# Performance work log

Hardware: AMD Instinct MI355X
Metric: run time of the kernel (lower is better)

Reference implementation:

```python
import jax, jax.numpy as jnp
import numpy as np

B, C, F_IN, F_HID, F_OUT = 256, 4096, 160, 192, 1
EPS = 1e-5


def setup_inputs() -> dict:
    key = jax.random.key(0)
    k1, k2, k3 = jax.random.split(key, 3)
    x = jax.random.normal(k1, (B, C, F_IN), dtype=jnp.float32)
    # MultipleLinear init: N(0, sqrt(2/in_features))
    W1 = jax.random.normal(k2, (C, F_HID, F_IN), dtype=jnp.float32) * np.sqrt(2.0 / F_IN)
    gamma = jnp.ones((C, F_HID), dtype=jnp.float32)
    beta = jnp.zeros((C, F_HID), dtype=jnp.float32)
    W2 = jax.random.normal(k3, (C, F_OUT, F_HID), dtype=jnp.float32) * np.sqrt(2.0 / F_HID)
    b2 = jnp.zeros((C, F_OUT), dtype=jnp.float32)
    return {"x": x, "W1": W1, "gamma": gamma, "beta": beta, "W2": W2, "b2": b2}


def reference(x, W1, gamma, beta, W2, b2):
    # Per-cell grouped linear: [B,C,160] x [C,192,160] -> [B,C,192]
    h = jnp.einsum('bci,coi->bco', x, W1)
    # Training-mode batchnorm over the batch dim, per (cell, feature)
    mean = jnp.mean(h, axis=0)                      # [C,192]
    var = jnp.mean((h - mean) ** 2, axis=0)         # biased variance, [C,192]
    h = (h - mean) * jax.lax.rsqrt(var + EPS) * gamma + beta
    h = jax.nn.relu(h)
    # Final per-cell linear: [B,C,192] x [C,1,192] -> [B,C,1]
    return jnp.einsum('bch,coh->bco', h, W2) + b2
```

## Files before the change

kernel.cpp:

```cpp
#include <hip/hip_runtime.h>
#include <hip/hip_bf16.h>

#define B_DIM 256
#define C_DIM 4096
#define FIN   160
#define FHID  192
#define EPS   1e-5f

#define AST 40
#define BST 40

typedef short  short8  __attribute__((ext_vector_type(8)));
typedef float  floatx4 __attribute__((ext_vector_type(4)));

__device__ __forceinline__ short f2bs(float f) {
  __hip_bfloat16 h = __float2bfloat16(f);
  return *reinterpret_cast<short*>(&h);
}

__device__ __forceinline__ void cvt_store8(short* dst, const float4& v0, const float4& v1) {
  short8 s;
  s[0] = f2bs(v0.x); s[1] = f2bs(v0.y); s[2] = f2bs(v0.z); s[3] = f2bs(v0.w);
  s[4] = f2bs(v1.x); s[5] = f2bs(v1.y); s[6] = f2bs(v1.z); s[7] = f2bs(v1.w);
  *reinterpret_cast<short8*>(dst) = s;
}

__global__ __launch_bounds__(1024) void mlp_fused_kernel(
    const float* __restrict__ x,
    const float* __restrict__ W1,
    const float* __restrict__ gamma,
    const float* __restrict__ beta,
    const float* __restrict__ W2,
    const float* __restrict__ b2,
    float* __restrict__ out)
{
  const int c    = blockIdx.x;
  const int tid  = threadIdx.x;
  const int lane = tid & 63;
  const int wave = tid >> 6;
  const int wr   = wave >> 2;
  const int wc   = wave & 3;
  const int l15  = lane & 15;
  const int lg   = lane >> 4;

  __shared__ __align__(16) short Alds[B_DIM * AST];
  __shared__ __align__(16) short Blds[FHID * BST];
  __shared__ float psum[4][FHID];
  __shared__ float psq [4][FHID];
  __shared__ float scaleS[FHID];
  __shared__ float shiftS[FHID];
  __shared__ float w2S[FHID];
  __shared__ float rowp[4][B_DIM];

  const float* xc  = x  + (size_t)c * FIN;
  const float* w1c = W1 + (size_t)c * FHID * FIN;

  const int  arow = tid >> 2;
  const int  aq   = (tid & 3) * 8;
  const bool bact = tid < 768;

  float4 a0, a1, b0, b1;
  {
    const float* pa = xc + (size_t)arow * (C_DIM * FIN) + aq;
    a0 = *reinterpret_cast<const float4*>(pa);
    a1 = *reinterpret_cast<const float4*>(pa + 4);
    if (bact) {
      const float* pb = w1c + arow * FIN + aq;
      b0 = *reinterpret_cast<const float4*>(pb);
      b1 = *reinterpret_cast<const float4*>(pb + 4);
    }
  }

  floatx4 acc[4][3];
  #pragma unroll
  for (int mt = 0; mt < 4; ++mt)
    #pragma unroll
    for (int nt = 0; nt < 3; ++nt)
      acc[mt][nt] = (floatx4)(0.f);

  for (int kc = 0; kc < 5; ++kc) {
    cvt_store8(&Alds[arow * AST + aq], a0, a1);
    if (bact) cvt_store8(&Blds[arow * BST + aq], b0, b1);
    __syncthreads();

    if (kc < 4) {
      const int k0 = (kc + 1) * 32;
      const float* pa = xc + (size_t)arow * (C_DIM * FIN) + k0 + aq;
      a0 = *reinterpret_cast<const float4*>(pa);
      a1 = *reinterpret_cast<const float4*>(pa + 4);
      if (bact) {
        const float* pb = w1c + arow * FIN + k0 + aq;
        b0 = *reinterpret_cast<const float4*>(pb);
        b1 = *reinterpret_cast<const float4*>(pb + 4);
      }
    }

    short8 af[4], bf[3];
    #pragma unroll
    for (int mt = 0; mt < 4; ++mt) {
      const int row = wr * 64 + mt * 16 + l15;
      af[mt] = *reinterpret_cast<const short8*>(&Alds[row * AST + lg * 8]);
    }
    #pragma unroll
    for (int nt = 0; nt < 3; ++nt) {
      const int row = wc * 48 + nt * 16 + l15;
      bf[nt] = *reinterpret_cast<const short8*>(&Blds[row * BST + lg * 8]);
    }
    #pragma unroll
    for (int mt = 0; mt < 4; ++mt)
      #pragma unroll
      for (int nt = 0; nt < 3; ++nt)
        acc[mt][nt] = __builtin_amdgcn_mfma_f32_16x16x32_bf16(
            af[mt], bf[nt], acc[mt][nt], 0, 0, 0);
    __syncthreads();
  }

  #pragma unroll
  for (int nt = 0; nt < 3; ++nt) {
    float s = 0.f, q = 0.f;
    #pragma unroll
    for (int mt = 0; mt < 4; ++mt)
      #pragma unroll
      for (int r = 0; r < 4; ++r) {
        const float v = acc[mt][nt][r];
        s += v; q += v * v;
      }
    s += __shfl_xor(s, 16); q += __shfl_xor(q, 16);
    s += __shfl_xor(s, 32); q += __shfl_xor(q, 32);
    if (lg == 0) {
      const int col = wc * 48 + nt * 16 + l15;
      psum[wr][col] = s;
      psq [wr][col] = q;
    }
  }
  __syncthreads();

  if (tid < FHID) {
    const float s  = psum[0][tid] + psum[1][tid] + psum[2][tid] + psum[3][tid];
    const float q  = psq [0][tid] + psq [1][tid] + psq [2][tid] + psq [3][tid];
    const float mean = s * (1.f / 256.f);
    const float var  = q * (1.f / 256.f) - mean * mean;
    const float rstd = rsqrtf(var + EPS);
    const float sc   = rstd * gamma[(size_t)c * FHID + tid];
    scaleS[tid] = sc;
    shiftS[tid] = beta[(size_t)c * FHID + tid] - mean * sc;
    w2S[tid]    = W2[(size_t)c * FHID + tid];
  }
  __syncthreads();

  #pragma unroll
  for (int mt = 0; mt < 4; ++mt) {
    #pragma unroll
    for (int r = 0; r < 4; ++r) {
      float p = 0.f;
      #pragma unroll
      for (int nt = 0; nt < 3; ++nt) {
        const int col = wc * 48 + nt * 16 + l15;
        float v = acc[mt][nt][r] * scaleS[col] + shiftS[col];
        v = fmaxf(v, 0.f);
        p += v * w2S[col];
      }
      p += __shfl_xor(p, 1);
      p += __shfl_xor(p, 2);
      p += __shfl_xor(p, 4);
      p += __shfl_xor(p, 8);
      if (l15 == 0) {
        const int row = wr * 64 + mt * 16 + lg * 4 + r;
        rowp[wc][row] = p;
      }
    }
  }
  __syncthreads();

  if (tid < B_DIM) {
    const float o = rowp[0][tid] + rowp[1][tid] + rowp[2][tid] + rowp[3][tid] + b2[c];
    out[(size_t)tid * C_DIM + c] = o;
  }
}

extern "C" void kernel_launch(void* const* d_in, const int* in_sizes, int n_in,
                              void* d_out, int out_size, void* d_ws, size_t ws_size,
                              hipStream_t stream) {
  const float* x     = (const float*)d_in[0];
  const float* W1    = (const float*)d_in[1];
  const float* gamma = (const float*)d_in[2];
  const float* beta  = (const float*)d_in[3];
  const float* W2    = (const float*)d_in[4];
  const float* b2    = (const float*)d_in[5];
  float* out = (float*)d_out;
  mlp_fused_kernel<<<C_DIM, 1024, 0, stream>>>(x, W1, gamma, beta, W2, b2, out);
}
```

Before: 1.204 ms.

## Stage full K dimension in LDS with all global loads issued upfront

Adds a kernel variant that loads the entire 160-wide K slice of x and W1 for a cell into about 160 KB of dynamic LDS in one burst. Each thread issues 20 vector loads before converting to bf16, then runs all five MFMA k-steps without intermediate barriers. This aims to raise memory-level parallelism and remove the per-chunk sync/load serialization of the double-buffered loop. The cost is that the LDS footprint limits a CU to one 1024-thread block, where the old kernel could fit two. The old kernel is kept as a fallback if the shared-memory attribute or the launch fails.

New measurement: 1.207 ms. Within noise of the previous version (+0.2%).

```diff
diff --git a/kernel.cpp b/kernel.cpp
--- a/kernel.cpp
+++ b/kernel.cpp
@@ -7,9 +7,6 @@
 #define FHID  192
 #define EPS   1e-5f
 
-#define AST 40
-#define BST 40
-
 typedef short  short8  __attribute__((ext_vector_type(8)));
 typedef float  floatx4 __attribute__((ext_vector_type(4)));
 
@@ -25,7 +22,170 @@
   *reinterpret_cast<short8*>(dst) = s;
 }
 
-__global__ __launch_bounds__(1024) void mlp_fused_kernel(
+#define AST_BIG 168
+#define A_SH (B_DIM * AST_BIG)
+#define B_SH (FHID  * AST_BIG)
+#define SMEM_BYTES (A_SH*2 + B_SH*2 + (8*FHID + 3*FHID + 4*B_DIM)*4)
+
+__global__ __launch_bounds__(1024) void mlp_fused_big(
+    const float* __restrict__ x,
+    const float* __restrict__ W1,
+    const float* __restrict__ gamma,
+    const float* __restrict__ beta,
+    const float* __restrict__ W2,
+    const float* __restrict__ b2,
+    float* __restrict__ out)
+{
+  extern __shared__ __align__(16) char smem[];
+  short* Alds   = reinterpret_cast<short*>(smem);
+  short* Blds   = Alds + A_SH;
+  float* psum   = reinterpret_cast<float*>(smem + (size_t)(A_SH + B_SH) * 2);
+  float* psq    = psum + 4 * FHID;
+  float* scaleS = psq + 4 * FHID;
+  float* shiftS = scaleS + FHID;
+  float* w2S    = shiftS + FHID;
+  float* rowp   = w2S + FHID;
+
+  const int c    = blockIdx.x;
+  const int tid  = threadIdx.x;
+  const int lane = tid & 63;
+  const int wave = tid >> 6;
+  const int wr   = wave >> 2;
+  const int wc   = wave & 3;
+  const int l15  = lane & 15;
+  const int lg   = lane >> 4;
+
+  const float* xc  = x  + (size_t)c * FIN;
+  const float* w1c = W1 + (size_t)c * FHID * FIN;
+
+  const int  r    = tid >> 2;
+  const int  q    = tid & 3;
+  const bool bact = tid < 4 * FHID;
+
+  {
+    const float* pa = xc + (size_t)r * (C_DIM * FIN) + q * 8;
+    const float* pb = w1c + r * FIN + q * 8;
+
+    float4 av[10];
+    float4 bv[10];
+    #pragma unroll
+    for (int j = 0; j < 5; ++j) {
+      av[2*j]   = *reinterpret_cast<const float4*>(pa + j*32);
+      av[2*j+1] = *reinterpret_cast<const float4*>(pa + j*32 + 4);
+    }
+    if (bact) {
+      #pragma unroll
+      for (int j = 0; j < 5; ++j) {
+        bv[2*j]   = *reinterpret_cast<const float4*>(pb + j*32);
+        bv[2*j+1] = *reinterpret_cast<const float4*>(pb + j*32 + 4);
+      }
+    }
+    short* da = Alds + r * AST_BIG + q * 8;
+    #pragma unroll
+    for (int j = 0; j < 5; ++j) cvt_store8(da + j*32, av[2*j], av[2*j+1]);
+    if (bact) {
+      short* db = Blds + r * AST_BIG + q * 8;
+      #pragma unroll
+      for (int j = 0; j < 5; ++j) cvt_store8(db + j*32, bv[2*j], bv[2*j+1]);
+    }
+  }
+  __syncthreads();
+
+  floatx4 acc[4][3];
+  #pragma unroll
+  for (int mt = 0; mt < 4; ++mt)
+    #pragma unroll
+    for (int nt = 0; nt < 3; ++nt)
+      acc[mt][nt] = (floatx4)(0.f);
+
+  const short* aB = Alds + (wr * 64 + l15) * AST_BIG + lg * 8;
+  const short* bB = Blds + (wc * 48 + l15) * AST_BIG + lg * 8;
+
+  #pragma unroll
+  for (int kc = 0; kc < 5; ++kc) {
+    short8 af[4], bf[3];
+    #pragma unroll
+    for (int mt = 0; mt < 4; ++mt)
+      af[mt] = *reinterpret_cast<const short8*>(aB + mt * 16 * AST_BIG + kc * 32);
+    #pragma unroll
+    for (int nt = 0; nt < 3; ++nt)
+      bf[nt] = *reinterpret_cast<const short8*>(bB + nt * 16 * AST_BIG + kc * 32);
+    #pragma unroll
+    for (int mt = 0; mt < 4; ++mt)
+      #pragma unroll
+      for (int nt = 0; nt < 3; ++nt)
+        acc[mt][nt] = __builtin_amdgcn_mfma_f32_16x16x32_bf16(
+            af[mt], bf[nt], acc[mt][nt], 0, 0, 0);
+  }
+
+  #pragma unroll
+  for (int nt = 0; nt < 3; ++nt) {
+    float s = 0.f, qq = 0.f;
+    #pragma unroll
+    for (int mt = 0; mt < 4; ++mt)
+      #pragma unroll
+      for (int rr = 0; rr < 4; ++rr) {
+        const float v = acc[mt][nt][rr];
+        s += v; qq += v * v;
+      }
+    s += __shfl_xor(s, 16); qq += __shfl_xor(qq, 16);
+    s += __shfl_xor(s, 32); qq += __shfl_xor(qq, 32);
+    if (lg == 0) {
+      const int col = wc * 48 + nt * 16 + l15;
+      psum[wr * FHID + col] = s;
+      psq [wr * FHID + col] = qq;
+    }
+  }
+  __syncthreads();
+
+  if (tid < FHID) {
+    const float s  = psum[0*FHID + tid] + psum[1*FHID + tid] + psum[2*FHID + tid] + psum[3*FHID + tid];
+    const float qq = psq [0*FHID + tid] + psq [1*FHID + tid] + psq [2*FHID + tid] + psq [3*FHID + tid];
+    const float mean = s * (1.f / 256.f);
+    const float var  = qq * (1.f / 256.f) - mean * mean;
+    const float rstd = rsqrtf(var + EPS);
+    const float sc   = rstd * gamma[(size_t)c * FHID + tid];
+    scaleS[tid] = sc;
+    shiftS[tid] = beta[(size_t)c * FHID + tid] - mean * sc;
+    w2S[tid]    = W2[(size_t)c * FHID + tid];
+  }
+  __syncthreads();
+
+  #pragma unroll
+  for (int mt = 0; mt < 4; ++mt) {
+    #pragma unroll
+    for (int rr = 0; rr < 4; ++rr) {
+      float p = 0.f;
+      #pragma unroll
+      for (int nt = 0; nt < 3; ++nt) {
+        const int col = wc * 48 + nt * 16 + l15;
+        float v = acc[mt][nt][rr] * scaleS[col] + shiftS[col];
+        v = fmaxf(v, 0.f);
+        p += v * w2S[col];
+      }
+      p += __shfl_xor(p, 1);
+      p += __shfl_xor(p, 2);
+      p += __shfl_xor(p, 4);
+      p += __shfl_xor(p, 8);
+      if (l15 == 0) {
+        const int row = wr * 64 + mt * 16 + lg * 4 + rr;
+        rowp[wc * B_DIM + row] = p;
+      }
+    }
+  }
+  __syncthreads();
+
+  if (tid < B_DIM) {
+    const float o = rowp[0*B_DIM + tid] + rowp[1*B_DIM + tid]
+                  + rowp[2*B_DIM + tid] + rowp[3*B_DIM + tid] + b2[c];
+    out[(size_t)tid * C_DIM + c] = o;
+  }
+}
+
+#define AST 40
+#define BST 40
+
+__global__ __launch_bounds__(1024) void mlp_fused_small(
     const float* __restrict__ x,
     const float* __restrict__ W1,
     const float* __restrict__ gamma,
@@ -117,29 +277,29 @@
 
   #pragma unroll
   for (int nt = 0; nt < 3; ++nt) {
-    float s = 0.f, q = 0.f;
-    #pragma unroll
-    for (int mt = 0; mt < 4; ++mt)
-      #pragma unroll
-      for (int r = 0; r < 4; ++r) {
-        const float v = acc[mt][nt][r];
-        s += v; q += v * v;
-      }
-    s += __shfl_xor(s, 16); q += __shfl_xor(q, 16);
-    s += __shfl_xor(s, 32); q += __shfl_xor(q, 32);
+    float s = 0.f, qv = 0.f;
+    #pragma unroll
+    for (int mt = 0; mt < 4; ++mt)
+      #pragma unroll
+      for (int rr = 0; rr < 4; ++rr) {
+        const float v = acc[mt][nt][rr];
+        s += v; qv += v * v;
+      }
+    s += __shfl_xor(s, 16); qv += __shfl_xor(qv, 16);
+    s += __shfl_xor(s, 32); qv += __shfl_xor(qv, 32);
     if (lg == 0) {
       const int col = wc * 48 + nt * 16 + l15;
       psum[wr][col] = s;
-      psq [wr][col] = q;
+      psq [wr][col] = qv;
     }
   }
   __syncthreads();
 
   if (tid < FHID) {
     const float s  = psum[0][tid] + psum[1][tid] + psum[2][tid] + psum[3][tid];
-    const float q  = psq [0][tid] + psq [1][tid] + psq [2][tid] + psq [3][tid];
+    const float qv = psq [0][tid] + psq [1][tid] + psq [2][tid] + psq [3][tid];
     const float mean = s * (1.f / 256.f);
-    const float var  = q * (1.f / 256.f) - mean * mean;
+    const float var  = qv * (1.f / 256.f) - mean * mean;
     const float rstd = rsqrtf(var + EPS);
     const float sc   = rstd * gamma[(size_t)c * FHID + tid];
     scaleS[tid] = sc;
@@ -151,12 +311,12 @@
   #pragma unroll
   for (int mt = 0; mt < 4; ++mt) {
     #pragma unroll
-    for (int r = 0; r < 4; ++r) {
+    for (int rr = 0; rr < 4; ++rr) {
       float p = 0.f;
       #pragma unroll
       for (int nt = 0; nt < 3; ++nt) {
         const int col = wc * 48 + nt * 16 + l15;
-        float v = acc[mt][nt][r] * scaleS[col] + shiftS[col];
+        float v = acc[mt][nt][rr] * scaleS[col] + shiftS[col];
         v = fmaxf(v, 0.f);
         p += v * w2S[col];
       }
@@ -165,7 +325,7 @@
       p += __shfl_xor(p, 4);
       p += __shfl_xor(p, 8);
       if (l15 == 0) {
-        const int row = wr * 64 + mt * 16 + lg * 4 + r;
+        const int row = wr * 64 + mt * 16 + lg * 4 + rr;
         rowp[wc][row] = p;
       }
     }
@@ -188,5 +348,19 @@
   const float* W2    = (const float*)d_in[4];
   const float* b2    = (const float*)d_in[5];
   float* out = (float*)d_out;
-  mlp_fused_kernel<<<C_DIM, 1024, 0, stream>>>(x, W1, gamma, beta, W2, b2, out);
-}
+
+  static int use_big = -1;
+  if (use_big < 0) {
+    use_big = (hipFuncSetAttribute(reinterpret_cast<const void*>(mlp_fused_big),
+                                   hipFuncAttributeMaxDynamicSharedMemorySize,
+                                   SMEM_BYTES) == hipSuccess) ? 1 : 0;
+  }
+  if (use_big) {
+    (void)hipGetLastError();
+    mlp_fused_big<<<C_DIM, 1024, SMEM_BYTES, stream>>>(x, W1, gamma, beta, W2, b2, out);
+    if (hipGetLastError() != hipSuccess) use_big = 0;
+  }
+  if (!use_big) {
+    mlp_fused_small<<<C_DIM, 1024, 0, stream>>>(x, W1, gamma, beta, W2, b2, out);
+  }
+}
```
